# Kernel optimization log

Measured on AMD Instinct MI355X. Metric: run time of the kernel, lower is better.

Reference implementation:

```python
import jax, jax.numpy as jnp
import numpy as np

B, N, D, H = 8, 1024, 768, 12
HD = D // H
SCALE = HD ** -0.5

def setup_inputs() -> dict:
    key = jax.random.key(0)
    k1, k2, k3, k4 = jax.random.split(key, 4)
    x = jax.random.normal(k1, (B, N, D), dtype=jnp.float32)
    weight = jax.random.uniform(k2, (B, N), dtype=jnp.float32)
    W_qkv = jax.random.normal(k3, (D, 3 * D), dtype=jnp.float32) * (D ** -0.5)
    W_msa = jax.random.normal(k4, (D, D), dtype=jnp.float32) * (D ** -0.5)
    b_msa = jnp.zeros((D,), dtype=jnp.float32)
    return {"x": x, "weight": weight, "W_qkv": W_qkv, "W_msa": W_msa, "b_msa": b_msa}

def reference(x, weight, W_qkv, W_msa, b_msa):
    # QKV projection (no bias), then elementwise per-token gate
    qkv = jnp.einsum('bnd,de->bne', x, W_qkv)          # [B,N,3D]
    qkv = weight[:, :, None] * qkv
    qkv = qkv.reshape(B, N, 3, H, HD).transpose(2, 0, 3, 1, 4)  # [3,B,H,N,hd]
    q, k, v = qkv[0], qkv[1], qkv[2]
    A = jnp.einsum('bhnd,bhmd->bhnm', q, k) * SCALE    # [B,H,N,N]
    A = jax.nn.softmax(A, axis=-1)
    out = jnp.einsum('bhnm,bhmd->bhnd', A, v)          # [B,H,N,hd]
    out = out.transpose(0, 2, 1, 3).reshape(B, N, D)
    return jnp.einsum('bnd,de->bne', out, W_msa) + b_msa
```

## Files before the change

kernel.cpp:

```cpp
#include <hip/hip_runtime.h>
#include <hip/hip_bf16.h>


typedef __attribute__((ext_vector_type(8))) short bf8;
typedef __attribute__((ext_vector_type(4))) float f4;

#define QSCALE 0.1803368801111204f
#define MFMA16 __builtin_amdgcn_mfma_f32_16x16x32_bf16

static __device__ __forceinline__ short bf16_of(float f) {
    union { float f; unsigned u; } a; a.f = f;
    unsigned r = a.u + 0x7FFFu + ((a.u >> 16) & 1u);
    return (short)(r >> 16);
}

static __device__ __forceinline__ unsigned bfpk(float lo, float hi) {
    float2 t; t.x = lo; t.y = hi;
    __hip_bfloat162 b = __float22bfloat162_rn(t);
    union { __hip_bfloat162 b; unsigned u; } c; c.b = b;
    return c.u;
}

static __device__ __forceinline__ void async16(const short* g, short* l) {
    __builtin_amdgcn_global_load_lds(
        (const __attribute__((address_space(1))) void*)g,
        (__attribute__((address_space(3))) void*)l, 16, 0, 0);
}

static __device__ __forceinline__ void transpose64(
        const float* __restrict__ w, short* __restrict__ wt,
        int K, int E, int k0, int e0, int tid, short (*t)[65]) {
#pragma unroll
    for (int p = 0; p < 16; ++p) {
        int idx = p * 256 + tid;
        int r = idx >> 6, c = idx & 63;
        t[r][c] = bf16_of(w[(k0 + r) * E + e0 + c]);
    }
    __syncthreads();
#pragma unroll
    for (int p = 0; p < 16; ++p) {
        int idx = p * 256 + tid;
        int r = idx >> 6, c = idx & 63;
        wt[(e0 + r) * K + k0 + c] = t[c][r];
    }
}

__global__ __launch_bounds__(256) void k_prep(
        const float* __restrict__ x, const float* __restrict__ gate,
        short* __restrict__ xb,
        const float* __restrict__ Wqkv, short* __restrict__ wtq,
        const float* __restrict__ Wmsa, short* __restrict__ wtm) {
    __shared__ short t[64][65];
    const int bid = blockIdx.x, tid = threadIdx.x;
    if (bid < 3072) {
        int i = bid * 256 + tid;
        const float g = gate[i / 96];
        const f4* sp = (const f4*)x;
        f4 a = sp[2 * i], b = sp[2 * i + 1];
        union { bf8 v; short h[8]; } o;
        o.h[0] = bf16_of(a[0] * g); o.h[1] = bf16_of(a[1] * g);
        o.h[2] = bf16_of(a[2] * g); o.h[3] = bf16_of(a[3] * g);
        o.h[4] = bf16_of(b[0] * g); o.h[5] = bf16_of(b[1] * g);
        o.h[6] = bf16_of(b[2] * g); o.h[7] = bf16_of(b[3] * g);
        ((bf8*)xb)[i] = o.v;
    } else if (bid < 3504) {
        int tt = bid - 3072;
        transpose64(Wqkv, wtq, 768, 2304, (tt / 36) * 64, (tt % 36) * 64, tid, t);
    } else {
        int tt = bid - 3504;
        transpose64(Wmsa, wtm, 768, 768, (tt / 12) * 64, (tt % 12) * 64, tid, t);
    }
}

static __device__ __forceinline__ void gemm128(const short* __restrict__ gA,
                                               const short* __restrict__ gB,
                                               short* smem,
                                               f4 acc[4][4]) {
    const int tid = threadIdx.x, lane = tid & 63;
    const int l16 = lane & 15, quad = lane >> 4, rx = l16 & 7;
    const int wm = (tid >> 6) & 1, wn = tid >> 7;

    auto stage = [&](short* S, int k0) {
#pragma unroll
        for (int c = 0; c < 4; ++c) {
            int p = c * 256 + tid;
            int row = p >> 3, slot = p & 7;
            int gc = slot ^ (row & 7);
            async16(gA + row * 768 + k0 + gc * 8, S + p * 8);
            async16(gB + row * 768 + k0 + gc * 8, S + 8192 + p * 8);
        }
    };

    stage(smem, 0);
    for (int it = 0; it < 12; ++it) {
        __builtin_amdgcn_s_waitcnt(0);
        __syncthreads();
        short* Sc = smem + (it & 1) * 16384;
        if (it + 1 < 12) stage(smem + ((it + 1) & 1) * 16384, (it + 1) * 64);
        const short* As = Sc;
        const short* Bs = Sc + 8192;
#pragma unroll
        for (int ks = 0; ks < 2; ++ks) {
            bf8 af[4], bfr[4];
#pragma unroll
            for (int mt = 0; mt < 4; ++mt)
                af[mt] = *(const bf8*)(As + (wm * 64 + mt * 16 + l16) * 64 +
                                       (((ks * 4 + quad) ^ rx) * 8));
#pragma unroll
            for (int nt = 0; nt < 4; ++nt)
                bfr[nt] = *(const bf8*)(Bs + (wn * 64 + nt * 16 + l16) * 64 +
                                        (((ks * 4 + quad) ^ rx) * 8));
#pragma unroll
            for (int mt = 0; mt < 4; ++mt)
#pragma unroll
                for (int nt = 0; nt < 4; ++nt)
                    acc[mt][nt] = MFMA16(af[mt], bfr[nt], acc[mt][nt], 0, 0, 0);
        }
    }
    __syncthreads();
}

__global__ __launch_bounds__(512, 2) void k_gemm_qkv(
        const short* __restrict__ xb, const short* __restrict__ wtq,
        short* __restrict__ qb, short* __restrict__ kb, short* __restrict__ vt) {
    __shared__ short lds[79872];
    const int tid = threadIdx.x, lane = tid & 63;
    const int l16 = lane & 15, quad = lane >> 4, rx = l16 & 7;
    const int wv = tid >> 6, wm = wv >> 1, wn = wv & 1;

    const int wg = blockIdx.x;
    const int swz = (wg & 7) * 64 + (wg >> 3);
    const int mI = swz >> 3, nI = swz & 7;
    const int m0 = mI * 128, n0 = nI * 288;

    const short* gA = xb + m0 * 768;
    const short* gB = wtq + n0 * 768;

    auto stageA = [&](int buf, int k0) {
        short* base = lds + buf * 26624;
#pragma unroll
        for (int j = 0; j < 2; ++j) {
            int p = j * 512 + tid, row = p >> 3;
            int gc = (p & 7) ^ (row & 7);
            async16(gA + row * 768 + k0 + gc * 8, base + p * 8);
        }
    };
    auto stageB = [&](int buf, int k0) {
        short* base = lds + buf * 26624 + 8192;
#pragma unroll
        for (int j = 0; j < 4; ++j) {
            int p = j * 512 + tid, row = p >> 3;
            int gc = (p & 7) ^ (row & 7);
            async16(gB + row * 768 + k0 + gc * 8, base + p * 8);
        }
        if (tid < 256) {
            int p = 2048 + tid, row = p >> 3;
            int gc = (p & 7) ^ (row & 7);
            async16(gB + row * 768 + k0 + gc * 8, base + p * 8);
        }
    };

    auto rdA = [&](const short* base, int mf, int ks) {
        return *(const bf8*)(base + (wm * 32 + mf * 16 + l16) * 64 +
                             (((ks * 4 + quad) ^ rx) << 3));
    };
    auto rdB = [&](const short* base, int nf, int ks) {
        return *(const bf8*)(base + 8192 + (wn * 144 + nf * 16 + l16) * 64 +
                             (((ks * 4 + quad) ^ rx) << 3));
    };

    f4 z = {0.f, 0.f, 0.f, 0.f};
    f4 acc[2][9];
#pragma unroll
    for (int mf = 0; mf < 2; ++mf)
#pragma unroll
        for (int nf = 0; nf < 9; ++nf) acc[mf][nf] = z;

    stageA(0, 0); stageB(0, 0);
    stageA(1, 64); stageB(1, 64);
    if (wv < 4) asm volatile("s_waitcnt vmcnt(7)" ::: "memory");
    else        asm volatile("s_waitcnt vmcnt(6)" ::: "memory");
    __builtin_amdgcn_s_barrier();

#pragma unroll 3
    for (int t = 0; t < 12; ++t) {
        const short* cur = lds + (t % 3) * 26624;
        bf8 af[2][2];
        af[0][0] = rdA(cur, 0, 0); af[0][1] = rdA(cur, 0, 1);
        af[1][0] = rdA(cur, 1, 0); af[1][1] = rdA(cur, 1, 1);
        bf8 bfr[5][2];
#pragma unroll
        for (int nf = 0; nf < 5; ++nf) { bfr[nf][0] = rdB(cur, nf, 0); bfr[nf][1] = rdB(cur, nf, 1); }
        if (t < 10) stageA((t + 2) % 3, (t + 2) * 64);
        __builtin_amdgcn_s_setprio(1);
#pragma unroll
        for (int mf = 0; mf < 2; ++mf)
#pragma unroll
            for (int nf = 0; nf < 5; ++nf) {
                acc[mf][nf] = MFMA16(af[mf][0], bfr[nf][0], acc[mf][nf], 0, 0, 0);
                acc[mf][nf] = MFMA16(af[mf][1], bfr[nf][1], acc[mf][nf], 0, 0, 0);
            }
        __builtin_amdgcn_s_setprio(0);
        bf8 bfh[4][2];
#pragma unroll
        for (int nf = 0; nf < 4; ++nf) { bfh[nf][0] = rdB(cur, nf + 5, 0); bfh[nf][1] = rdB(cur, nf + 5, 1); }
        if (t < 10) stageB((t + 2) % 3, (t + 2) * 64);
        __builtin_amdgcn_s_setprio(1);
#pragma unroll
        for (int mf = 0; mf < 2; ++mf)
#pragma unroll
            for (int nf = 0; nf < 4; ++nf) {
                acc[mf][nf + 5] = MFMA16(af[mf][0], bfh[nf][0], acc[mf][nf + 5], 0, 0, 0);
                acc[mf][nf + 5] = MFMA16(af[mf][1], bfh[nf][1], acc[mf][nf + 5], 0, 0, 0);
            }
        __builtin_amdgcn_s_setprio(0);
        if (t < 10) {
            if (wv < 4) asm volatile("s_waitcnt vmcnt(7)" ::: "memory");
            else        asm volatile("s_waitcnt vmcnt(6)" ::: "memory");
            __builtin_amdgcn_s_barrier();
        } else if (t == 10) {
            asm volatile("s_waitcnt vmcnt(0)" ::: "memory");
            __builtin_amdgcn_s_barrier();
        }
    }

    const int bI = m0 >> 10, nn0 = m0 & 1023;
#pragma unroll
    for (int nf = 0; nf < 9; ++nf) {
        const int ct = n0 + wn * 144 + nf * 16;
        if (ct < 1536) {
            const int which = (ct >= 768) ? 1 : 0;
            const int h = (ct - which * 768) >> 6;
            const int hd = (ct & 63) + l16;
            short* dst = (which ? kb : qb) + (bI * 12 + h) * 65536 + hd;
#pragma unroll
            for (int mf = 0; mf < 2; ++mf)
#pragma unroll
                for (int r = 0; r < 4; ++r) {
                    const int nn = nn0 + wm * 32 + mf * 16 + quad * 4 + r;
                    const float val = acc[mf][nf][r];
                    dst[nn * 64] = bf16_of(which ? val : val * QSCALE);
                }
        }
    }
    const int vstart = (n0 >= 1536) ? n0 : 1536;
    const int npass = (n0 + 288 > vstart) ? (n0 + 288 - vstart) / 96 : 0;
    for (int p = 0; p < npass; ++p) {
        __syncthreads();
        const int c0 = vstart + p * 96;
#pragma unroll
        for (int nf = 0; nf < 9; ++nf) {
            const int ct = n0 + wn * 144 + nf * 16;
            if (ct >= c0 && ct < c0 + 96) {
                const int lc = ct - c0 + l16;
#pragma unroll
                for (int mf = 0; mf < 2; ++mf)
#pragma unroll
                    for (int r = 0; r < 4; ++r) {
                        const int rl = wm * 32 + mf * 16 + quad * 4 + r;
                        lds[lc * 136 + rl] = bf16_of(acc[mf][nf][r]);
                    }
            }
        }
        __syncthreads();
        const int vg0 = c0 - 1536;
#pragma unroll
        for (int u = 0; u < 3; ++u) {
            const int idx = u * 512 + tid;
            const int lc = idx >> 4, ck = idx & 15;
            const int vg = vg0 + lc;
            const int h = vg >> 6, hd = vg & 63;
            bf8 vv = *(const bf8*)(lds + lc * 136 + ck * 8);
            *(bf8*)(vt + ((bI * 12 + h) * 64 + hd) * 1024 + nn0 + ck * 8) = vv;
        }
    }
}

__global__ __launch_bounds__(256) void k_gemm_final(
        const short* __restrict__ attn, const short* __restrict__ wtm,
        const float* __restrict__ bias, float* __restrict__ out) {
    __shared__ short smem[32768];
    const int lane = threadIdx.x & 63;
    const int l16 = lane & 15, quad = lane >> 4;
    const int wm = (threadIdx.x >> 6) & 1, wn = threadIdx.x >> 7;
    const int m0 = blockIdx.y * 128, n0 = blockIdx.x * 128;
    f4 z = {0.f, 0.f, 0.f, 0.f};
    f4 acc[4][4] = {{z,z,z,z},{z,z,z,z},{z,z,z,z},{z,z,z,z}};
    gemm128(attn + m0 * 768, wtm + n0 * 768, smem, acc);
#pragma unroll
    for (int mt = 0; mt < 4; ++mt) {
#pragma unroll
        for (int r = 0; r < 4; ++r) {
            const int row = m0 + wm * 64 + mt * 16 + quad * 4 + r;
#pragma unroll
            for (int nt = 0; nt < 4; ++nt) {
                const int e = n0 + wn * 64 + nt * 16 + l16;
                out[row * 768 + e] = acc[mt][nt][r] + bias[e];
            }
        }
    }
}

__global__ __launch_bounds__(256, 3) void k_attn(const short* __restrict__ qb,
                                                 const short* __restrict__ kb,
                                                 const short* __restrict__ vt,
                                                 short* __restrict__ attn) {
    __shared__ short Ks[2][4096];
    __shared__ short Vs[2][4096];
    const int tid = threadIdx.x, wave = tid >> 6, lane = tid & 63;
    const int l16 = lane & 15, quad = lane >> 4;
    const int bh = blockIdx.x;
    const int b = bh / 12, h = bh - b * 12;
    const int m_base = blockIdx.y * 128 + wave * 32;
    const short* qh = qb + bh * 65536;
    const short* kh = kb + bh * 65536;
    const short* vh = vt + bh * 65536;

    const int rA = ((l16 >> 2) << 3) + (l16 & 3);
    const int fK = (((rA >> 3) & 1) << 2) + (rA & 3);
    const int sK = (quad ^ fK) * 8;
    const int oAlo = rA * 64 + sK;
    const int oAhi = rA * 64 + (sK ^ 32);
    const int oBlo = oAlo + 256, oBhi = oAhi + 256;
    const int fV = (((l16 >> 3) & 1) << 2) + (l16 & 3);
    const int oV = l16 * 64 + ((quad ^ fV) * 8);

    const short* qp0 = qh + (m_base + l16) * 64 + quad * 8;
    bf8 qf00 = *(const bf8*)(qp0);
    bf8 qf01 = *(const bf8*)(qp0 + 32);
    const short* qp1 = qp0 + 16 * 64;
    bf8 qf10 = *(const bf8*)(qp1);
    bf8 qf11 = *(const bf8*)(qp1 + 32);

    union { bf8 v; short h[8]; } onef;
#pragma unroll
    for (int i = 0; i < 8; ++i) onef.h[i] = (short)0x3F80;

    f4 z = {0.f, 0.f, 0.f, 0.f};
    f4 acc0[4] = {z, z, z, z};
    f4 acc1[4] = {z, z, z, z};
    f4 accl0 = z, accl1 = z;

    auto stage = [&](int buf, int j0) {
#pragma unroll
        for (int j = 0; j < 2; ++j) {
            int idx = j * 256 + tid;
            int row = idx >> 3;
            int fr = (((row >> 3) & 1) << 2) + (row & 3);
            int gc = (idx & 7) ^ fr;
            async16(kh + (j0 + row) * 64 + gc * 8, Ks[buf] + idx * 8);
            async16(vh + row * 1024 + j0 + gc * 8, Vs[buf] + idx * 8);
        }
    };

    stage(0, 0);
    int cur = 0;
    for (int it = 0; it < 16; ++it) {
        __builtin_amdgcn_s_waitcnt(0);
        __syncthreads();
        if (it + 1 < 16) stage(cur ^ 1, (it + 1) * 64);
        const short* Kc = Ks[cur];
        const short* Vc = Vs[cur];

#pragma unroll
        for (int jj = 0; jj < 64; jj += 32) {
            const short* kjj = Kc + jj * 64;
            bf8 kAlo = *(const bf8*)(kjj + oAlo);
            bf8 kAhi = *(const bf8*)(kjj + oAhi);
            bf8 kBlo = *(const bf8*)(kjj + oBlo);
            bf8 kBhi = *(const bf8*)(kjj + oBhi);
            bf8 vf0 = *(const bf8*)(Vc + 0 * 1024 + (oV ^ (jj ? 32 : 0)));
            bf8 vf1 = *(const bf8*)(Vc + 1 * 1024 + (oV ^ (jj ? 32 : 0)));
            bf8 vf2 = *(const bf8*)(Vc + 2 * 1024 + (oV ^ (jj ? 32 : 0)));
            bf8 vf3 = *(const bf8*)(Vc + 3 * 1024 + (oV ^ (jj ? 32 : 0)));

            {
                f4 sA = z, sB = z;
                sA = MFMA16(kAlo, qf00, sA, 0, 0, 0);
                sA = MFMA16(kAhi, qf01, sA, 0, 0, 0);
                sB = MFMA16(kBlo, qf00, sB, 0, 0, 0);
                sB = MFMA16(kBhi, qf01, sB, 0, 0, 0);
                float a0 = __builtin_amdgcn_exp2f(sA[0]);
                float a1 = __builtin_amdgcn_exp2f(sA[1]);
                float a2 = __builtin_amdgcn_exp2f(sA[2]);
                float a3 = __builtin_amdgcn_exp2f(sA[3]);
                float b0 = __builtin_amdgcn_exp2f(sB[0]);
                float b1 = __builtin_amdgcn_exp2f(sB[1]);
                float b2 = __builtin_amdgcn_exp2f(sB[2]);
                float b3 = __builtin_amdgcn_exp2f(sB[3]);
                union { bf8 v; unsigned u[4]; } p;
                p.u[0] = bfpk(a0, a1); p.u[1] = bfpk(a2, a3);
                p.u[2] = bfpk(b0, b1); p.u[3] = bfpk(b2, b3);
                accl0 = MFMA16(onef.v, p.v, accl0, 0, 0, 0);
                acc0[0] = MFMA16(vf0, p.v, acc0[0], 0, 0, 0);
                acc0[1] = MFMA16(vf1, p.v, acc0[1], 0, 0, 0);
                acc0[2] = MFMA16(vf2, p.v, acc0[2], 0, 0, 0);
                acc0[3] = MFMA16(vf3, p.v, acc0[3], 0, 0, 0);
            }
            {
                f4 sA = z, sB = z;
                sA = MFMA16(kAlo, qf10, sA, 0, 0, 0);
                sA = MFMA16(kAhi, qf11, sA, 0, 0, 0);
                sB = MFMA16(kBlo, qf10, sB, 0, 0, 0);
                sB = MFMA16(kBhi, qf11, sB, 0, 0, 0);
                float a0 = __builtin_amdgcn_exp2f(sA[0]);
                float a1 = __builtin_amdgcn_exp2f(sA[1]);
                float a2 = __builtin_amdgcn_exp2f(sA[2]);
                float a3 = __builtin_amdgcn_exp2f(sA[3]);
                float b0 = __builtin_amdgcn_exp2f(sB[0]);
                float b1 = __builtin_amdgcn_exp2f(sB[1]);
                float b2 = __builtin_amdgcn_exp2f(sB[2]);
                float b3 = __builtin_amdgcn_exp2f(sB[3]);
                union { bf8 v; unsigned u[4]; } p;
                p.u[0] = bfpk(a0, a1); p.u[1] = bfpk(a2, a3);
                p.u[2] = bfpk(b0, b1); p.u[3] = bfpk(b2, b3);
                accl1 = MFMA16(onef.v, p.v, accl1, 0, 0, 0);
                acc1[0] = MFMA16(vf0, p.v, acc1[0], 0, 0, 0);
                acc1[1] = MFMA16(vf1, p.v, acc1[1], 0, 0, 0);
                acc1[2] = MFMA16(vf2, p.v, acc1[2], 0, 0, 0);
                acc1[3] = MFMA16(vf3, p.v, acc1[3], 0, 0, 0);
            }
        }
        cur ^= 1;
    }

    const float inv0 = 1.f / accl0[0];
    const float inv1 = 1.f / accl1[0];
    const int row0 = (b << 10) + m_base + l16;
    short* op0 = attn + row0 * 768 + h * 64 + quad * 4;
    short* op1 = op0 + 16 * 768;
#pragma unroll
    for (int dt = 0; dt < 4; ++dt)
#pragma unroll
        for (int r = 0; r < 4; ++r) {
            op0[dt * 16 + r] = bf16_of(acc0[dt][r] * inv0);
            op1[dt * 16 + r] = bf16_of(acc1[dt][r] * inv1);
        }
}

extern "C" void kernel_launch(void* const* d_in, const int* in_sizes, int n_in,
                              void* d_out, int out_size, void* d_ws, size_t ws_size,
                              hipStream_t stream) {
    const float* x    = (const float*)d_in[0];
    const float* gate = (const float*)d_in[1];
    const float* Wqkv = (const float*)d_in[2];
    const float* Wmsa = (const float*)d_in[3];
    const float* bmsa = (const float*)d_in[4];
    float* out = (float*)d_out;

    char* ws = (char*)d_ws;
    short* xb  = (short*)(ws);
    short* wtq = (short*)(ws + 12582912);
    short* wtm = (short*)(ws + 16121856);
    short* qb  = (short*)(ws + 17301504);
    short* kb  = (short*)(ws + 29884416);
    short* vt  = (short*)(ws + 42467328);
    short* attn = xb;

    k_prep<<<3648, 256, 0, stream>>>(x, gate, xb, Wqkv, wtq, Wmsa, wtm);
    k_gemm_qkv<<<512, 512, 0, stream>>>(xb, wtq, qb, kb, vt);
    k_attn<<<dim3(96, 8), 256, 0, stream>>>(qb, kb, vt, attn);
    k_gemm_final<<<dim3(6, 64), 256, 0, stream>>>(attn, wtm, bmsa, out);
}
```

Before: 186.5 us.

## Shrink QKV GEMM tile to 128x144 with 4 waves and double buffering

Halves the QKV GEMM block tile from 128x288 (8 waves) to 128x144 (4 waves), doubling the grid to 1024 blocks. The three-stage LDS ring with staggered vmcnt waits becomes a two-stage double buffer that waits for all loads each iteration. The smaller LDS footprint allows more resident blocks per CU, but each block gets less B-operand reuse and there is less overlap between loads and MFMA work. The V-transpose epilogue passes are resized to match.

```diff
diff --git a/kernel.cpp b/kernel.cpp
--- a/kernel.cpp
+++ b/kernel.cpp
@@ -120,41 +120,41 @@
     __syncthreads();
 }
 
-__global__ __launch_bounds__(512, 2) void k_gemm_qkv(
+__global__ __launch_bounds__(256, 2) void k_gemm_qkv(
         const short* __restrict__ xb, const short* __restrict__ wtq,
         short* __restrict__ qb, short* __restrict__ kb, short* __restrict__ vt) {
-    __shared__ short lds[79872];
+    __shared__ short lds[34816];
     const int tid = threadIdx.x, lane = tid & 63;
     const int l16 = lane & 15, quad = lane >> 4, rx = l16 & 7;
-    const int wv = tid >> 6, wm = wv >> 1, wn = wv & 1;
+    const int wm = tid >> 6;
 
     const int wg = blockIdx.x;
-    const int swz = (wg & 7) * 64 + (wg >> 3);
-    const int mI = swz >> 3, nI = swz & 7;
-    const int m0 = mI * 128, n0 = nI * 288;
+    const int swz = (wg & 7) * 128 + (wg >> 3);
+    const int mI = swz >> 4, nI = swz & 15;
+    const int m0 = mI * 128, n0 = nI * 144;
 
     const short* gA = xb + m0 * 768;
     const short* gB = wtq + n0 * 768;
 
     auto stageA = [&](int buf, int k0) {
-        short* base = lds + buf * 26624;
-#pragma unroll
-        for (int j = 0; j < 2; ++j) {
-            int p = j * 512 + tid, row = p >> 3;
+        short* base = lds + buf * 17408;
+#pragma unroll
+        for (int j = 0; j < 4; ++j) {
+            int p = j * 256 + tid, row = p >> 3;
             int gc = (p & 7) ^ (row & 7);
             async16(gA + row * 768 + k0 + gc * 8, base + p * 8);
         }
     };
     auto stageB = [&](int buf, int k0) {
-        short* base = lds + buf * 26624 + 8192;
+        short* base = lds + buf * 17408 + 8192;
 #pragma unroll
         for (int j = 0; j < 4; ++j) {
-            int p = j * 512 + tid, row = p >> 3;
+            int p = j * 256 + tid, row = p >> 3;
             int gc = (p & 7) ^ (row & 7);
             async16(gB + row * 768 + k0 + gc * 8, base + p * 8);
         }
-        if (tid < 256) {
-            int p = 2048 + tid, row = p >> 3;
+        if (tid < 128) {
+            int p = 1024 + tid, row = p >> 3;
             int gc = (p & 7) ^ (row & 7);
             async16(gB + row * 768 + k0 + gc * 8, base + p * 8);
         }
@@ -165,7 +165,7 @@
                              (((ks * 4 + quad) ^ rx) << 3));
     };
     auto rdB = [&](const short* base, int nf, int ks) {
-        return *(const bf8*)(base + 8192 + (wn * 144 + nf * 16 + l16) * 64 +
+        return *(const bf8*)(base + 8192 + (nf * 16 + l16) * 64 +
                              (((ks * 4 + quad) ^ rx) << 3));
     };
 
@@ -177,21 +177,19 @@
         for (int nf = 0; nf < 9; ++nf) acc[mf][nf] = z;
 
     stageA(0, 0); stageB(0, 0);
-    stageA(1, 64); stageB(1, 64);
-    if (wv < 4) asm volatile("s_waitcnt vmcnt(7)" ::: "memory");
-    else        asm volatile("s_waitcnt vmcnt(6)" ::: "memory");
+    asm volatile("s_waitcnt vmcnt(0)" ::: "memory");
     __builtin_amdgcn_s_barrier();
 
-#pragma unroll 3
+#pragma unroll 2
     for (int t = 0; t < 12; ++t) {
-        const short* cur = lds + (t % 3) * 26624;
+        const short* cur = lds + (t & 1) * 17408;
         bf8 af[2][2];
         af[0][0] = rdA(cur, 0, 0); af[0][1] = rdA(cur, 0, 1);
         af[1][0] = rdA(cur, 1, 0); af[1][1] = rdA(cur, 1, 1);
         bf8 bfr[5][2];
 #pragma unroll
         for (int nf = 0; nf < 5; ++nf) { bfr[nf][0] = rdB(cur, nf, 0); bfr[nf][1] = rdB(cur, nf, 1); }
-        if (t < 10) stageA((t + 2) % 3, (t + 2) * 64);
+        if (t < 11) stageA((t + 1) & 1, (t + 1) * 64);
         __builtin_amdgcn_s_setprio(1);
 #pragma unroll
         for (int mf = 0; mf < 2; ++mf)
@@ -204,7 +202,7 @@
         bf8 bfh[4][2];
 #pragma unroll
         for (int nf = 0; nf < 4; ++nf) { bfh[nf][0] = rdB(cur, nf + 5, 0); bfh[nf][1] = rdB(cur, nf + 5, 1); }
-        if (t < 10) stageB((t + 2) % 3, (t + 2) * 64);
+        if (t < 11) stageB((t + 1) & 1, (t + 1) * 64);
         __builtin_amdgcn_s_setprio(1);
 #pragma unroll
         for (int mf = 0; mf < 2; ++mf)
@@ -214,20 +212,14 @@
                 acc[mf][nf + 5] = MFMA16(af[mf][1], bfh[nf][1], acc[mf][nf + 5], 0, 0, 0);
             }
         __builtin_amdgcn_s_setprio(0);
-        if (t < 10) {
-            if (wv < 4) asm volatile("s_waitcnt vmcnt(7)" ::: "memory");
-            else        asm volatile("s_waitcnt vmcnt(6)" ::: "memory");
-            __builtin_amdgcn_s_barrier();
-        } else if (t == 10) {
-            asm volatile("s_waitcnt vmcnt(0)" ::: "memory");
-            __builtin_amdgcn_s_barrier();
-        }
+        asm volatile("s_waitcnt vmcnt(0)" ::: "memory");
+        __builtin_amdgcn_s_barrier();
     }
 
     const int bI = m0 >> 10, nn0 = m0 & 1023;
 #pragma unroll
     for (int nf = 0; nf < 9; ++nf) {
-        const int ct = n0 + wn * 144 + nf * 16;
+        const int ct = n0 + nf * 16;
         if (ct < 1536) {
             const int which = (ct >= 768) ? 1 : 0;
             const int h = (ct - which * 768) >> 6;
@@ -243,22 +235,23 @@
                 }
         }
     }
-    const int vstart = (n0 >= 1536) ? n0 : 1536;
-    const int npass = (n0 + 288 > vstart) ? (n0 + 288 - vstart) / 96 : 0;
+    const int vlo = (n0 >= 1536) ? n0 : 1536;
+    const int vcnt = n0 + 144 - vlo;
+    const int npass = (vcnt > 0) ? vcnt / 48 : 0;
     for (int p = 0; p < npass; ++p) {
         __syncthreads();
-        const int c0 = vstart + p * 96;
+        const int c0 = vlo + p * 48;
 #pragma unroll
         for (int nf = 0; nf < 9; ++nf) {
-            const int ct = n0 + wn * 144 + nf * 16;
-            if (ct >= c0 && ct < c0 + 96) {
-                const int lc = ct - c0 + l16;
+            const int ct = n0 + nf * 16;
+            if (ct >= c0 && ct < c0 + 48) {
+                const int lcol = ct - c0 + l16;
 #pragma unroll
                 for (int mf = 0; mf < 2; ++mf)
 #pragma unroll
                     for (int r = 0; r < 4; ++r) {
-                        const int rl = wm * 32 + mf * 16 + quad * 4 + r;
-                        lds[lc * 136 + rl] = bf16_of(acc[mf][nf][r]);
+                        const int row = wm * 32 + mf * 16 + quad * 4 + r;
+                        lds[lcol * 136 + row] = bf16_of(acc[mf][nf][r]);
                     }
             }
         }
@@ -266,7 +259,7 @@
         const int vg0 = c0 - 1536;
 #pragma unroll
         for (int u = 0; u < 3; ++u) {
-            const int idx = u * 512 + tid;
+            const int idx = u * 256 + tid;
             const int lc = idx >> 4, ck = idx & 15;
             const int vg = vg0 + lc;
             const int h = vg >> 6, hd = vg & 63;
@@ -458,7 +451,7 @@
     short* attn = xb;
 
     k_prep<<<3648, 256, 0, stream>>>(x, gate, xb, Wqkv, wtq, Wmsa, wtm);
-    k_gemm_qkv<<<512, 512, 0, stream>>>(xb, wtq, qb, kb, vt);
+    k_gemm_qkv<<<1024, 256, 0, stream>>>(xb, wtq, qb, kb, vt);
     k_attn<<<dim3(96, 8), 256, 0, stream>>>(qb, kb, vt, attn);
     k_gemm_final<<<dim3(6, 64), 256, 0, stream>>>(attn, wtm, bmsa, out);
 }
```

New measurement: 178.3 us. 4.4% less time.
